# Optimization experiments

Hardware: AMD Instinct MI355X
Metric: run time of the kernel (lower is better)

## Reference

```python
import jax, jax.numpy as jnp
import numpy as np

B, H, S, F, D = 16, 8, 512, 512, 64
RANK = 12
TOPK_RATIO = 0.1
LN_EPS = 1e-5


def _layernorm(x, w, b):
    mu = jnp.mean(x, axis=-1, keepdims=True)
    var = jnp.mean((x - mu) ** 2, axis=-1, keepdims=True)
    return (x - mu) * jax.lax.rsqrt(var + LN_EPS) * w + b


def _topk_mask(logits, k):
    # keep top-k along last axis, set the rest to -inf (torch topk+scatter equivalent)
    vals, _ = jax.lax.top_k(logits, k)
    kth = vals[..., -1:]
    return jnp.where(logits >= kth, logits, -jnp.inf)


def setup_inputs() -> dict:
    key = jax.random.key(0)
    ks = jax.random.split(key, 4)
    values = jax.random.normal(ks[0], (B, F, H, D), dtype=jnp.float32)
    # stand-in for per-head orthogonal init (rows ~ unit norm scale)
    alpha = jax.random.normal(ks[1], (H, S, F), dtype=jnp.float32) / np.float32(np.sqrt(F))
    temp = jnp.ones((H, 1), dtype=jnp.float32)
    gamma_hs = jnp.zeros((H, S, 1), dtype=jnp.float32)
    U = jax.random.normal(ks[2], (H, S, RANK), dtype=jnp.float32) * 0.01
    V = jax.random.normal(ks[3], (H, RANK, F), dtype=jnp.float32) * 0.01
    ln_w = jnp.ones((F,), dtype=jnp.float32)
    ln_b = jnp.zeros((F,), dtype=jnp.float32)
    return {"values": values, "alpha": alpha, "temp": temp, "gamma_hs": gamma_hs,
            "U": U, "V": V, "ln_w": ln_w, "ln_b": ln_b}


def reference(values, alpha, temp, gamma_hs, U, V, ln_w, ln_b):
    scale = np.float32(1.0 / np.sqrt(F))
    alpha_logits = (alpha * scale)[None]                      # [1,H,S,F]

    # data logits from value energies
    w = jnp.transpose(values, (0, 2, 1, 3))                    # [B,H,F,D]
    energy = jnp.mean(w * w, axis=-1)                          # [B,H,F]
    rms = jnp.maximum(jnp.sqrt(jnp.mean(energy, axis=-1, keepdims=True)), 1e-6)
    score = energy / rms                                       # [B,H,F]
    gain = jax.nn.softplus(temp)[:, 0]                         # [H]
    score = score * gain[None, :, None]
    score = _layernorm(score, ln_w, ln_b)                      # LN over F
    bilinear = jnp.einsum('hsr,hrf->hsf', U, V)                # [H,S,F]
    data_logits = score[:, :, None, :] + gamma_hs[None] + bilinear[None]  # [B,H,S,F]

    k = max(1, int(TOPK_RATIO * F))
    data_logits = _topk_mask(data_logits, k)
    alpha_logits = _topk_mask(alpha_logits, k)

    attn_mix = jax.nn.softmax(data_logits, axis=-1) + jax.nn.softmax(alpha_logits, axis=-1)
    out = jnp.einsum('bhsf,bfhd->bshd', attn_mix, values)      # [B,S,H,D]
    return out
```

## Files before the change

kernel.cpp:

```cpp
#include <hip/hip_runtime.h>
#include <math.h>

#define BB 16
#define HH 8
#define SS 512
#define FF 512
#define DD 64
#define RANKK 12
#define KTOP 51
#define ROWS 8

typedef __attribute__((ext_vector_type(8))) short bf16x8;
typedef __attribute__((ext_vector_type(4))) float f32x4;

__device__ __forceinline__ unsigned short f2bf(float x){
  unsigned u = __float_as_uint(x);
  return (unsigned short)((u + 0x7FFFu + ((u>>16)&1u)) >> 16);
}
__device__ __forceinline__ float bf2f(unsigned short h){
  return __uint_as_float(((unsigned)h)<<16);
}

__device__ __forceinline__ unsigned f2ord(float x){
  unsigned u = __float_as_uint(x);
  return (u & 0x80000000u) ? ~u : (u | 0x80000000u);
}

__device__ __forceinline__ void topk_softmax8(float (&a)[8]){
  unsigned key[8];
#pragma unroll
  for (int j=0;j<8;++j) key[j] = f2ord(a[j]);
  unsigned T = 0u;
#pragma unroll
  for (int bit=31; bit>=0; --bit){
    unsigned Tp = T | (1u<<bit);
    int cnt = 0;
#pragma unroll
    for (int j=0;j<8;++j){
      unsigned long long bl = __ballot(key[j] >= Tp);
      cnt += __popcll(bl);
    }
    if (cnt >= KTOP) T = Tp;
    if (cnt == KTOP) break;
  }
  float m = a[0];
#pragma unroll
  for (int j=1;j<8;++j) m = fmaxf(m, a[j]);
#pragma unroll
  for (int off=32; off>=1; off>>=1) m = fmaxf(m, __shfl_xor(m, off));
  float sum = 0.f;
#pragma unroll
  for (int j=0;j<8;++j){
    float e = (key[j] >= T) ? expf(a[j]-m) : 0.f;
    a[j] = e; sum += e;
  }
#pragma unroll
  for (int off=32; off>=1; off>>=1) sum += __shfl_xor(sum, off);
  float inv = 1.f/sum;
#pragma unroll
  for (int j=0;j<8;++j) a[j] *= inv;
}

__global__ __launch_bounds__(512) void k_score(const float* __restrict__ values,
    const float* __restrict__ temp, const float* __restrict__ ln_w,
    const float* __restrict__ ln_b, float* __restrict__ score_ln)
{
  const int b = blockIdx.x / HH, h = blockIdx.x % HH;
  const int tid = threadIdx.x, w = tid >> 6, lane = tid & 63;
  __shared__ float s_e[FF];
  __shared__ float ps[8], ps2[8];
  const float* vb = values + ((size_t)b*FF*HH + h)*DD;
  for (int i=0;i<FF/8;++i){
    int f = w*(FF/8) + i;
    float v = vb[(size_t)f*HH*DD + lane];
    float e = v*v;
#pragma unroll
    for (int off=32; off>=1; off>>=1) e += __shfl_xor(e, off);
    if (lane==0) s_e[f] = e * (1.0f/DD);
  }
  __syncthreads();
  float e = s_e[tid];
  float se = e, se2 = e*e;
#pragma unroll
  for (int off=32; off>=1; off>>=1){ se += __shfl_xor(se, off); se2 += __shfl_xor(se2, off); }
  if (lane==0){ ps[w]=se; ps2[w]=se2; }
  __syncthreads();
  float S1=0.f, S2=0.f;
#pragma unroll
  for (int g=0; g<8; ++g){ S1 += ps[g]; S2 += ps2[g]; }
  float meanE = S1 * (1.0f/FF);
  float rms = fmaxf(sqrtf(meanE), 1e-6f);
  float t = temp[h];
  float gain = (t > 20.f) ? t : log1pf(expf(t));
  float c = gain / rms;
  float mu = c * meanE;
  float var = c*c*(S2*(1.0f/FF) - meanE*meanE);
  float inv = rsqrtf(var + 1e-5f);
  score_ln[(size_t)blockIdx.x*FF + tid] = (c*e - mu)*inv*ln_w[tid] + ln_b[tid];
}

__global__ __launch_bounds__(512) void k_alpha(const float* __restrict__ alpha,
                                               float* __restrict__ A_soft)
{
  const int w = threadIdx.x >> 6, lane = threadIdx.x & 63;
  const int row = blockIdx.x * ROWS + w;
  const float SCALE = (float)(1.0/sqrt((double)FF));
  const float* ar = alpha + (size_t)row*FF + lane*8;
  float4 v0 = *(const float4*)ar;
  float4 v1 = *(const float4*)(ar+4);
  float a[8] = {v0.x*SCALE, v0.y*SCALE, v0.z*SCALE, v0.w*SCALE,
                v1.x*SCALE, v1.y*SCALE, v1.z*SCALE, v1.w*SCALE};
  topk_softmax8(a);
  float* orow = A_soft + (size_t)row*FF + lane*8;
  *(float4*)orow     = make_float4(a[0],a[1],a[2],a[3]);
  *(float4*)(orow+4) = make_float4(a[4],a[5],a[6],a[7]);
}

__global__ __launch_bounds__(512) void k_prep_t(const float* __restrict__ values,
    unsigned short* __restrict__ hiP, unsigned short* __restrict__ loP, int b0)
{
  const int bloc_h = blockIdx.x;
  const int b = b0 + bloc_h / HH, h = bloc_h % HH;
  const int tid = threadIdx.x, w = tid >> 6, lane = tid & 63;
  __shared__ float tile[64][65];
  const float* vb = values + ((size_t)b*FF*HH + h)*DD;
  for (int c=0;c<8;++c){
#pragma unroll
    for (int p=0;p<8;++p){
      const int fi = p*8 + w;
      const int f  = c*64 + fi;
      tile[fi][lane] = vb[(size_t)f*HH*DD + lane];
    }
    __syncthreads();
    {
      const int d  = w*8 + (lane>>3);
      const int fj = (lane&7)*8;
      unsigned short hs[8], ls[8];
#pragma unroll
      for (int j=0;j<8;++j){
        float x = tile[fj+j][d];
        hs[j] = f2bf(x);
        ls[j] = f2bf(x - bf2f(hs[j]));
      }
      uint4 H4, L4;
      H4.x=(unsigned)hs[0]|((unsigned)hs[1]<<16); H4.y=(unsigned)hs[2]|((unsigned)hs[3]<<16);
      H4.z=(unsigned)hs[4]|((unsigned)hs[5]<<16); H4.w=(unsigned)hs[6]|((unsigned)hs[7]<<16);
      L4.x=(unsigned)ls[0]|((unsigned)ls[1]<<16); L4.y=(unsigned)ls[2]|((unsigned)ls[3]<<16);
      L4.z=(unsigned)ls[4]|((unsigned)ls[5]<<16); L4.w=(unsigned)ls[6]|((unsigned)ls[7]<<16);
      const size_t base = ((size_t)bloc_h*DD + d)*FF + c*64 + fj;
      *(uint4*)(hiP + base) = H4;
      *(uint4*)(loP + base) = L4;
    }
    __syncthreads();
  }
}

__device__ __forceinline__ void build_mix_row(int bh, int h, int s, int lane,
    const float* __restrict__ score_ln, const float* __restrict__ gamma,
    const float* __restrict__ U, const float* __restrict__ V,
    const float* __restrict__ A_soft, float4& m0, float4& m1)
{
  const int f0 = lane*8;
  const float* sr = score_ln + (size_t)bh*FF + f0;
  float4 sv0 = *(const float4*)sr;
  float4 sv1 = *(const float4*)(sr+4);
  const float g = gamma[h*SS + s];
  float dl[8] = {sv0.x+g, sv0.y+g, sv0.z+g, sv0.w+g,
                 sv1.x+g, sv1.y+g, sv1.z+g, sv1.w+g};
  const float* Ur = U + ((size_t)h*SS + s)*RANKK;
  const float* Vh = V + (size_t)h*RANKK*FF + f0;
#pragma unroll
  for (int r=0;r<RANKK;++r){
    float u = Ur[r];
    float4 b0 = *(const float4*)(Vh + r*FF);
    float4 b1 = *(const float4*)(Vh + r*FF + 4);
    dl[0] += u*b0.x; dl[1] += u*b0.y; dl[2] += u*b0.z; dl[3] += u*b0.w;
    dl[4] += u*b1.x; dl[5] += u*b1.y; dl[6] += u*b1.z; dl[7] += u*b1.w;
  }
  topk_softmax8(dl);
  const float* arow = A_soft + ((size_t)h*SS + s)*FF + f0;
  float4 a0 = *(const float4*)arow;
  float4 a1 = *(const float4*)(arow+4);
  m0 = make_float4(dl[0]+a0.x, dl[1]+a0.y, dl[2]+a0.z, dl[3]+a0.w);
  m1 = make_float4(dl[4]+a1.x, dl[5]+a1.y, dl[6]+a1.z, dl[7]+a1.w);
}

__device__ __forceinline__ void gload16(const void* g, void* l){
  __builtin_amdgcn_global_load_lds(
      (const __attribute__((address_space(1))) unsigned int*)g,
      (__attribute__((address_space(3))) unsigned int*)l, 16, 0, 0);
}

#define VMCNT1 asm volatile("s_waitcnt vmcnt(1)" ::: "memory")
#define VMCNT0 asm volatile("s_waitcnt vmcnt(0)" ::: "memory")
#define LGKM0  asm volatile("s_waitcnt lgkmcnt(0)" ::: "memory")
#define MEMFENCE asm volatile("" ::: "memory")

template<int NB>
__global__ __launch_bounds__(512, 4) void k_mfma_t(
    const unsigned short* __restrict__ hiP, const unsigned short* __restrict__ loP,
    const float* __restrict__ gamma, const float* __restrict__ U,
    const float* __restrict__ V, const float* __restrict__ score_ln,
    const float* __restrict__ A_soft, float* __restrict__ out, int b0)
{
  __shared__ __align__(16) unsigned char Abuf[65536];
  __shared__ __align__(16) unsigned char Bbuf[2][8192];
  const int nwg = HH*NB*16;
  const int bid = (blockIdx.x & 7)*(nwg/8) + (blockIdx.x >> 3);
  const int grp  = bid >> 4;
  const int sblk = bid & 15;
  const int h    = grp / NB;
  const int bloc = grp % NB;
  const int b    = b0 + bloc;
  const int s0   = sblk*32;
  const int bh   = b*HH + h;
  const int tid = threadIdx.x, w = tid>>6, lane = tid&63;

  const size_t pbBase = (size_t)(bloc*HH + h)*DD*FF;
  const int dw  = tid >> 3;
  const int s8p = tid & 7;
  const int s8  = s8p ^ (dw & 7);
  const unsigned short* sp = ((s8 & 4) ? loP : hiP)
                             + pbBase + (size_t)dw*FF + (size_t)(s8 & 3)*8;
  gload16(sp, &Bbuf[0][(unsigned)w<<10]);

#pragma unroll
  for (int i=0;i<4;++i){
    const int sl = w*4 + i;
    float4 m0, m1;
    build_mix_row(bh, h, s0+sl, lane, score_ln, gamma, U, V, A_soft, m0, m1);
    float xs[8] = {m0.x,m0.y,m0.z,m0.w,m1.x,m1.y,m1.z,m1.w};
    unsigned short hs[8], ls[8];
#pragma unroll
    for (int j=0;j<8;++j){
      hs[j] = f2bf(xs[j]);
      ls[j] = f2bf(xs[j] - bf2f(hs[j]));
    }
    uint4 H4, L4;
    H4.x = (unsigned)hs[0] | ((unsigned)hs[1]<<16);
    H4.y = (unsigned)hs[2] | ((unsigned)hs[3]<<16);
    H4.z = (unsigned)hs[4] | ((unsigned)hs[5]<<16);
    H4.w = (unsigned)hs[6] | ((unsigned)hs[7]<<16);
    L4.x = (unsigned)ls[0] | ((unsigned)ls[1]<<16);
    L4.y = (unsigned)ls[2] | ((unsigned)ls[3]<<16);
    L4.z = (unsigned)ls[4] | ((unsigned)ls[5]<<16);
    L4.w = (unsigned)ls[6] | ((unsigned)ls[7]<<16);
    const unsigned byt = (unsigned)(sl*1024 + lane*16) ^ (unsigned)((sl&15)<<4);
    *(uint4*)(Abuf + byt)          = H4;
    *(uint4*)(Abuf + 32768 + byt)  = L4;
  }
  __syncthreads();

  const int stile = w>>2, ntile = w&3;
  const int srow  = stile*16 + (lane&15);
  const unsigned sw = (unsigned)((lane&15)<<4);
  const unsigned a0off = (unsigned)(srow*1024 + ((lane>>4)*16));
  const int d    = ntile*16 + (lane&15);
  const int sgr  = lane>>4;
  const unsigned offH = (unsigned)(d*128 + ((sgr    ) ^ (d&7))*16);
  const unsigned offL = (unsigned)(d*128 + ((sgr + 4) ^ (d&7))*16);

  f32x4 acc0 = {0.f,0.f,0.f,0.f};
  f32x4 acc1 = {0.f,0.f,0.f,0.f};

#pragma unroll
  for (int t=0;t<16;++t){
    if (t < 15){
      gload16(sp + (size_t)(t+1)*32, &Bbuf[(t+1)&1][(unsigned)w<<10]);
      VMCNT1;
    } else {
      VMCNT0;
    }
    __builtin_amdgcn_s_barrier();
    MEMFENCE;
    const unsigned ax = (a0off + (unsigned)(t*64)) ^ sw;
    bf16x8 ah = *(const bf16x8*)(Abuf + ax);
    bf16x8 al = *(const bf16x8*)(Abuf + 32768 + ax);
    const unsigned char* bb = Bbuf[t&1];
    bf16x8 bhv = *(const bf16x8*)(bb + offH);
    bf16x8 blv = *(const bf16x8*)(bb + offL);
    acc0 = __builtin_amdgcn_mfma_f32_16x16x32_bf16(ah, bhv, acc0, 0, 0, 0);
    acc1 = __builtin_amdgcn_mfma_f32_16x16x32_bf16(al, bhv, acc1, 0, 0, 0);
    acc1 = __builtin_amdgcn_mfma_f32_16x16x32_bf16(ah, blv, acc1, 0, 0, 0);
    if (t < 15){
      LGKM0;
      __builtin_amdgcn_s_barrier();
      MEMFENCE;
    }
  }

  const int m0r = stile*16 + (lane>>4)*4;
#pragma unroll
  for (int r=0;r<4;++r){
    const int s = s0 + m0r + r;
    __builtin_nontemporal_store(acc0[r] + acc1[r],
        &out[(((size_t)b*SS + s)*HH + h)*DD + d]);
  }
}

__global__ __launch_bounds__(512) void k_main_lds(const float* __restrict__ values,
    const float* __restrict__ alpha, const float* __restrict__ gamma,
    const float* __restrict__ U, const float* __restrict__ V,
    const float* __restrict__ score_ln, float* __restrict__ out)
{
  const int nwg = BB*HH*(SS/ROWS);
  const int bid = (blockIdx.x & 7)*(nwg/8) + (blockIdx.x >> 3);
  const int blocksPerBH = SS / ROWS;
  const int bh = bid / blocksPerBH;
  const int s0 = (bid % blocksPerBH) * ROWS;
  const int b = bh / HH, h = bh % HH;
  const int tid = threadIdx.x, w = tid >> 6, lane = tid & 63;
  __shared__ float smix[ROWS][FF];

  {
    const int s = s0 + w;
    const int f0 = lane*8;
    const float* sr = score_ln + (size_t)bh*FF + f0;
    float4 sv0 = *(const float4*)sr;
    float4 sv1 = *(const float4*)(sr+4);
    const float g = gamma[h*SS + s];
    float dl[8] = {sv0.x+g, sv0.y+g, sv0.z+g, sv0.w+g,
                   sv1.x+g, sv1.y+g, sv1.z+g, sv1.w+g};
    const float* Ur = U + ((size_t)h*SS + s)*RANKK;
    const float* Vh = V + (size_t)h*RANKK*FF + f0;
#pragma unroll
    for (int r=0;r<RANKK;++r){
      float u = Ur[r];
      float4 b0 = *(const float4*)(Vh + r*FF);
      float4 b1 = *(const float4*)(Vh + r*FF + 4);
      dl[0] += u*b0.x; dl[1] += u*b0.y; dl[2] += u*b0.z; dl[3] += u*b0.w;
      dl[4] += u*b1.x; dl[5] += u*b1.y; dl[6] += u*b1.z; dl[7] += u*b1.w;
    }
    topk_softmax8(dl);
    const float SCALE = (float)(1.0/sqrt((double)FF));
    const float* arow = alpha + ((size_t)h*SS + s)*FF + f0;
    float4 a0 = *(const float4*)arow;
    float4 a1 = *(const float4*)(arow+4);
    float ap[8] = {a0.x*SCALE, a0.y*SCALE, a0.z*SCALE, a0.w*SCALE,
                   a1.x*SCALE, a1.y*SCALE, a1.z*SCALE, a1.w*SCALE};
    topk_softmax8(ap);
    float4 m0 = make_float4(dl[0]+ap[0], dl[1]+ap[1], dl[2]+ap[2], dl[3]+ap[3]);
    float4 m1 = make_float4(dl[4]+ap[4], dl[5]+ap[5], dl[6]+ap[6], dl[7]+ap[7]);
    *(float4*)&smix[w][f0]   = m0;
    *(float4*)&smix[w][f0+4] = m1;
  }
  __syncthreads();

  float acc[ROWS] = {0,0,0,0,0,0,0,0};
  {
    const float* vp = values + (size_t)b*FF*HH*DD + (size_t)h*DD + lane;
#pragma unroll
    for (int i=0;i<16;++i){
      const int f0 = w*64 + i*4;
      float x0 = vp[(size_t)(f0+0)*HH*DD];
      float x1 = vp[(size_t)(f0+1)*HH*DD];
      float x2 = vp[(size_t)(f0+2)*HH*DD];
      float x3 = vp[(size_t)(f0+3)*HH*DD];
#pragma unroll
      for (int r=0;r<ROWS;++r){
        float4 m = *(const float4*)&smix[r][f0];
        acc[r] += m.x*x0 + m.y*x1 + m.z*x2 + m.w*x3;
      }
    }
  }
  __syncthreads();

  float* red = &smix[0][0];
#pragma unroll
  for (int r=0;r<ROWS;++r) red[(w*ROWS + r)*64 + lane] = acc[r];
  __syncthreads();
  {
    const int r = w, dd = lane;
    float sum = 0.f;
#pragma unroll
    for (int g=0; g<8; ++g) sum += red[(g*ROWS + r)*64 + dd];
    out[(((size_t)b*SS + s0 + r)*HH + h)*DD + dd] = sum;
  }
}

extern "C" void kernel_launch(void* const* d_in, const int* in_sizes, int n_in,
                              void* d_out, int out_size, void* d_ws, size_t ws_size,
                              hipStream_t stream) {
  const float* values = (const float*)d_in[0];
  const float* alpha  = (const float*)d_in[1];
  const float* temp   = (const float*)d_in[2];
  const float* gamma  = (const float*)d_in[3];
  const float* U      = (const float*)d_in[4];
  const float* V      = (const float*)d_in[5];
  const float* ln_w   = (const float*)d_in[6];
  const float* ln_b   = (const float*)d_in[7];
  float* out = (float*)d_out;
  float* ws  = (float*)d_ws;

  const size_t scoreN = (size_t)BB*HH*FF;
  const size_t alphaN = (size_t)HH*SS*FF;
  const size_t planeFull = (size_t)BB*HH*DD*FF;
  const size_t planeHalf = planeFull/2;

  float* score_ln = ws;
  float* A_soft   = ws + scoreN;
  unsigned short* hiP = (unsigned short*)(ws + scoreN + alphaN);

  const size_t baseB    = (scoreN + alphaN)*sizeof(float);
  const size_t needFull = baseB + 2*planeFull*sizeof(unsigned short);
  const size_t needHalf = baseB + 2*planeHalf*sizeof(unsigned short);

  hipLaunchKernelGGL(k_score, dim3(BB*HH), dim3(512), 0, stream,
                     values, temp, ln_w, ln_b, score_ln);
  if (ws_size >= needFull){
    unsigned short* loP = hiP + planeFull;
    hipLaunchKernelGGL(k_alpha, dim3(HH*SS/ROWS), dim3(512), 0, stream, alpha, A_soft);
    hipLaunchKernelGGL(k_prep_t, dim3(BB*HH), dim3(512), 0, stream, values, hiP, loP, 0);
    hipLaunchKernelGGL((k_mfma_t<BB>), dim3(HH*16*BB), dim3(512), 0, stream,
                       hiP, loP, gamma, U, V, score_ln, A_soft, out, 0);
  } else if (ws_size >= needHalf){
    unsigned short* loP = hiP + planeHalf;
    hipLaunchKernelGGL(k_alpha, dim3(HH*SS/ROWS), dim3(512), 0, stream, alpha, A_soft);
    for (int c=0;c<2;++c){
      hipLaunchKernelGGL(k_prep_t, dim3((BB/2)*HH), dim3(512), 0, stream,
                         values, hiP, loP, c*(BB/2));
      hipLaunchKernelGGL((k_mfma_t<BB/2>), dim3(HH*16*(BB/2)), dim3(512), 0, stream,
                         hiP, loP, gamma, U, V, score_ln, A_soft, out, c*(BB/2));
    }
  } else {
    hipLaunchKernelGGL(k_main_lds, dim3(BB*HH*(SS/ROWS)), dim3(512), 0, stream,
                       values, alpha, gamma, U, V, score_ln, out);
  }
}
```

Measured before the change: 181.9 us.

## Fuse score, alpha softmax and bf16 split prep into one kernel; restructure MFMA pipeline

Merges the three preprocessing kernels (score LayerNorm, alpha top-k softmax, hi/lo bf16 transpose of values) into a single launch, with extra blocks handling alpha rows. This removes two kernel launches and their serialization gaps. The MFMA loop's double-buffer sync is reduced to one barrier per iteration with a combined waitcnt, and MFMA issue is wrapped in raised wave priority. The single barrier now waits for the in-flight prefetch at the start of each step, which may expose load latency that the earlier vmcnt(1) scheme overlapped with compute.

```diff
diff --git a/kernel.cpp b/kernel.cpp
--- a/kernel.cpp
+++ b/kernel.cpp
@@ -59,6 +59,93 @@
   float inv = 1.f/sum;
 #pragma unroll
   for (int j=0;j<8;++j) a[j] *= inv;
+}
+
+__global__ __launch_bounds__(512) void k_prep_all(
+    const float* __restrict__ values, const float* __restrict__ temp,
+    const float* __restrict__ ln_w, const float* __restrict__ ln_b,
+    const float* __restrict__ alpha, float* __restrict__ score_ln,
+    unsigned short* __restrict__ hiP, unsigned short* __restrict__ loP,
+    float* __restrict__ A_soft)
+{
+  const int tid = threadIdx.x, w = tid >> 6, lane = tid & 63;
+  if (blockIdx.x >= BB*HH){
+    const int row = (int)(blockIdx.x - BB*HH) * ROWS + w;
+    const float SCALE = (float)(1.0/sqrt((double)FF));
+    const float* ar = alpha + (size_t)row*FF + lane*8;
+    float4 v0 = *(const float4*)ar;
+    float4 v1 = *(const float4*)(ar+4);
+    float a[8] = {v0.x*SCALE, v0.y*SCALE, v0.z*SCALE, v0.w*SCALE,
+                  v1.x*SCALE, v1.y*SCALE, v1.z*SCALE, v1.w*SCALE};
+    topk_softmax8(a);
+    float* orow = A_soft + (size_t)row*FF + lane*8;
+    *(float4*)orow     = make_float4(a[0],a[1],a[2],a[3]);
+    *(float4*)(orow+4) = make_float4(a[4],a[5],a[6],a[7]);
+    return;
+  }
+  __shared__ float tile[64][65];
+  __shared__ float s_e[FF];
+  __shared__ float ps[8], ps2[8];
+  const int b = blockIdx.x / HH, h = blockIdx.x % HH;
+  const float* vb = values + ((size_t)b*FF*HH + h)*DD;
+
+  for (int c=0;c<8;++c){
+#pragma unroll
+    for (int p=0;p<8;++p){
+      const int fi = p*8 + w;
+      const int f  = c*64 + fi;
+      tile[fi][lane] = vb[(size_t)f*HH*DD + lane];
+    }
+    __syncthreads();
+    {
+      const int d  = w*8 + (lane>>3);
+      const int fj = (lane&7)*8;
+      unsigned short hs[8], ls[8];
+#pragma unroll
+      for (int j=0;j<8;++j){
+        float x = tile[fj+j][d];
+        hs[j] = f2bf(x);
+        ls[j] = f2bf(x - bf2f(hs[j]));
+      }
+      uint4 H4, L4;
+      H4.x=(unsigned)hs[0]|((unsigned)hs[1]<<16); H4.y=(unsigned)hs[2]|((unsigned)hs[3]<<16);
+      H4.z=(unsigned)hs[4]|((unsigned)hs[5]<<16); H4.w=(unsigned)hs[6]|((unsigned)hs[7]<<16);
+      L4.x=(unsigned)ls[0]|((unsigned)ls[1]<<16); L4.y=(unsigned)ls[2]|((unsigned)ls[3]<<16);
+      L4.z=(unsigned)ls[4]|((unsigned)ls[5]<<16); L4.w=(unsigned)ls[6]|((unsigned)ls[7]<<16);
+      const size_t base = ((size_t)blockIdx.x*DD + d)*FF + c*64 + fj;
+      *(uint4*)(hiP + base) = H4;
+      *(uint4*)(loP + base) = L4;
+    }
+    __syncthreads();
+  }
+
+  for (int i=0;i<FF/8;++i){
+    int f = w*(FF/8) + i;
+    float v = vb[(size_t)f*HH*DD + lane];
+    float e = v*v;
+#pragma unroll
+    for (int off=32; off>=1; off>>=1) e += __shfl_xor(e, off);
+    if (lane==0) s_e[f] = e * (1.0f/DD);
+  }
+  __syncthreads();
+  float e = s_e[tid];
+  float se = e, se2 = e*e;
+#pragma unroll
+  for (int off=32; off>=1; off>>=1){ se += __shfl_xor(se, off); se2 += __shfl_xor(se2, off); }
+  if (lane==0){ ps[w]=se; ps2[w]=se2; }
+  __syncthreads();
+  float S1=0.f, S2=0.f;
+#pragma unroll
+  for (int g=0; g<8; ++g){ S1 += ps[g]; S2 += ps2[g]; }
+  float meanE = S1 * (1.0f/FF);
+  float rms = fmaxf(sqrtf(meanE), 1e-6f);
+  float t = temp[h];
+  float gain = (t > 20.f) ? t : log1pf(expf(t));
+  float c = gain / rms;
+  float mu = c * meanE;
+  float var = c*c*(S2*(1.0f/FF) - meanE*meanE);
+  float inv = rsqrtf(var + 1e-5f);
+  score_ln[(size_t)blockIdx.x*FF + tid] = (c*e - mu)*inv*ln_w[tid] + ln_b[tid];
 }
 
 __global__ __launch_bounds__(512) void k_score(const float* __restrict__ values,
@@ -191,11 +278,6 @@
       (__attribute__((address_space(3))) unsigned int*)l, 16, 0, 0);
 }
 
-#define VMCNT1 asm volatile("s_waitcnt vmcnt(1)" ::: "memory")
-#define VMCNT0 asm volatile("s_waitcnt vmcnt(0)" ::: "memory")
-#define LGKM0  asm volatile("s_waitcnt lgkmcnt(0)" ::: "memory")
-#define MEMFENCE asm volatile("" ::: "memory")
-
 template<int NB>
 __global__ __launch_bounds__(512, 4) void k_mfma_t(
     const unsigned short* __restrict__ hiP, const unsigned short* __restrict__ loP,
@@ -265,28 +347,23 @@
 
 #pragma unroll
   for (int t=0;t<16;++t){
-    if (t < 15){
+    if (t > 0){
+      asm volatile("s_waitcnt vmcnt(0) lgkmcnt(0)" ::: "memory");
+      __builtin_amdgcn_s_barrier();
+    }
+    if (t < 15)
       gload16(sp + (size_t)(t+1)*32, &Bbuf[(t+1)&1][(unsigned)w<<10]);
-      VMCNT1;
-    } else {
-      VMCNT0;
-    }
-    __builtin_amdgcn_s_barrier();
-    MEMFENCE;
     const unsigned ax = (a0off + (unsigned)(t*64)) ^ sw;
     bf16x8 ah = *(const bf16x8*)(Abuf + ax);
     bf16x8 al = *(const bf16x8*)(Abuf + 32768 + ax);
     const unsigned char* bb = Bbuf[t&1];
     bf16x8 bhv = *(const bf16x8*)(bb + offH);
     bf16x8 blv = *(const bf16x8*)(bb + offL);
+    __builtin_amdgcn_s_setprio(1);
     acc0 = __builtin_amdgcn_mfma_f32_16x16x32_bf16(ah, bhv, acc0, 0, 0, 0);
     acc1 = __builtin_amdgcn_mfma_f32_16x16x32_bf16(al, bhv, acc1, 0, 0, 0);
     acc1 = __builtin_amdgcn_mfma_f32_16x16x32_bf16(ah, blv, acc1, 0, 0, 0);
-    if (t < 15){
-      LGKM0;
-      __builtin_amdgcn_s_barrier();
-      MEMFENCE;
-    }
+    __builtin_amdgcn_s_setprio(0);
   }
 
   const int m0r = stile*16 + (lane>>4)*4;
@@ -405,16 +482,16 @@
   const size_t needFull = baseB + 2*planeFull*sizeof(unsigned short);
   const size_t needHalf = baseB + 2*planeHalf*sizeof(unsigned short);
 
-  hipLaunchKernelGGL(k_score, dim3(BB*HH), dim3(512), 0, stream,
-                     values, temp, ln_w, ln_b, score_ln);
   if (ws_size >= needFull){
     unsigned short* loP = hiP + planeFull;
-    hipLaunchKernelGGL(k_alpha, dim3(HH*SS/ROWS), dim3(512), 0, stream, alpha, A_soft);
-    hipLaunchKernelGGL(k_prep_t, dim3(BB*HH), dim3(512), 0, stream, values, hiP, loP, 0);
+    hipLaunchKernelGGL(k_prep_all, dim3(BB*HH + HH*SS/ROWS), dim3(512), 0, stream,
+                       values, temp, ln_w, ln_b, alpha, score_ln, hiP, loP, A_soft);
     hipLaunchKernelGGL((k_mfma_t<BB>), dim3(HH*16*BB), dim3(512), 0, stream,
                        hiP, loP, gamma, U, V, score_ln, A_soft, out, 0);
   } else if (ws_size >= needHalf){
     unsigned short* loP = hiP + planeHalf;
+    hipLaunchKernelGGL(k_score, dim3(BB*HH), dim3(512), 0, stream,
+                       values, temp, ln_w, ln_b, score_ln);
     hipLaunchKernelGGL(k_alpha, dim3(HH*SS/ROWS), dim3(512), 0, stream, alpha, A_soft);
     for (int c=0;c<2;++c){
       hipLaunchKernelGGL(k_prep_t, dim3((BB/2)*HH), dim3(512), 0, stream,
@@ -423,6 +500,8 @@
                          hiP, loP, gamma, U, V, score_ln, A_soft, out, c*(BB/2));
     }
   } else {
+    hipLaunchKernelGGL(k_score, dim3(BB*HH), dim3(512), 0, stream,
+                       values, temp, ln_w, ln_b, score_ln);
     hipLaunchKernelGGL(k_main_lds, dim3(BB*HH*(SS/ROWS)), dim3(512), 0, stream,
                        values, alpha, gamma, U, V, score_ln, out);
   }
```

Result: faster. 173.5 us (-4.6%).
